# Kernel optimization log

Measured on AMD Instinct MI355X. Metric: run time of the kernel, lower is better.

## Reference

```python
import jax, jax.numpy as jnp
import numpy as np

GRID = 1024   # grid side -> V = GRID^2 verts
BATCH = 8     # homogeneous batch of meshes


def _grid_mesh_faces(S):
    # Triangulated regular grid: 2 triangles per cell.
    idx = np.arange(S * S, dtype=np.int64).reshape(S, S)
    a = idx[:-1, :-1].ravel()
    b = a + 1
    c = a + S
    d = a + S + 1
    f1 = np.stack([a, b, c], axis=1)
    f2 = np.stack([b, d, c], axis=1)
    return np.concatenate([f1, f2], axis=0)  # (F, 3) int64


def _unique_edges(faces, V):
    # Edge k of a face is opposite vertex k (pytorch3d convention):
    # edges = [(v1,v2), (v0,v2), (v0,v1)]
    e = np.stack([faces[:, [1, 2]], faces[:, [0, 2]], faces[:, [0, 1]]], axis=1)  # (F,3,2)
    e = np.sort(e, axis=-1)
    keys = e[..., 0] * np.int64(V) + e[..., 1]
    uniq, inv = np.unique(keys.ravel(), return_inverse=True)
    edges = np.stack([uniq // V, uniq % V], axis=1).astype(np.int64)  # (E,2)
    face_to_edge = inv.reshape(-1, 3).astype(np.int64)                # (F,3)
    return edges, face_to_edge


def setup_inputs() -> dict:
    key = jax.random.key(0)
    V = GRID * GRID
    faces_np = _grid_mesh_faces(GRID)
    edges_np, fte_np = _unique_edges(faces_np, V)
    verts = jax.random.normal(key, (BATCH, V, 3), dtype=jnp.float32)
    return {
        "verts": verts,
        "faces": jnp.asarray(faces_np),
        "edges": jnp.asarray(edges_np),
        "face_to_edge": jnp.asarray(fte_np),
    }


def reference(verts, faces, edges, face_to_edge):
    # verts: (N, V, 3); faces: (F, 3); edges: (E, 2); face_to_edge: (F, 3)
    N, V, _ = verts.shape
    # Gather edge endpoints and average to midpoints: (N, E, 2, 3) -> (N, E, 3)
    mid = verts[:, edges].mean(axis=2)
    # New verts = original verts followed by edge midpoints
    new_verts = jnp.concatenate([verts, mid], axis=1)  # (N, V+E, 3)
    # New faces (pytorch3d SubdivideMeshes._subdivide_faces ordering):
    e = face_to_edge + V  # midpoint vertex indices
    f0 = jnp.stack([faces[:, 0], e[:, 2], e[:, 1]], axis=1)
    f1 = jnp.stack([faces[:, 1], e[:, 0], e[:, 2]], axis=1)
    f2 = jnp.stack([faces[:, 2], e[:, 1], e[:, 0]], axis=1)
    f3 = e
    new_faces = jnp.concatenate([f0, f1, f2, f3], axis=0)  # (4F, 3)
    return new_verts, new_faces
```

## Files before the change

### kernel.cpp

```cpp
#include <hip/hip_runtime.h>
#include <stdint.h>


#define GRID_S 1024
#define V_CONST (GRID_S * GRID_S)

typedef float f4v __attribute__((ext_vector_type(4)));
typedef float f2v __attribute__((ext_vector_type(2)));

__global__ void copy_verts_k(const float* __restrict__ verts,
                             float* __restrict__ out,
                             int perBatch,
                             int rowStride3) {
    const int n = blockIdx.y;
    const int d0 = n * rowStride3;
    const float* __restrict__ src = verts + n * perBatch;
    float* __restrict__ dst = out + d0;

    const int pad = (4 - (d0 & 3)) & 3;
    const int main4 = (perBatch - pad) >> 2;
    const int k = blockIdx.x * blockDim.x + threadIdx.x;

    if (k < main4) {
        const int s = pad + (k << 2);
        f4v v;
        if (pad == 0) {
            v = *reinterpret_cast<const f4v*>(src + s);
        } else {
            v[0] = src[s + 0];
            v[1] = src[s + 1];
            v[2] = src[s + 2];
            v[3] = src[s + 3];
        }
        __builtin_nontemporal_store(v, reinterpret_cast<f4v*>(dst + s));
    }
    if (k == 0) {
        const int rem = (perBatch - pad) & 3;
        for (int i = 0; i < pad; ++i) dst[i] = src[i];
        for (int i = perBatch - rem; i < perBatch; ++i) dst[i] = src[i];
    }
}

__global__ void midpoints_k(const float* __restrict__ verts,
                            const int2* __restrict__ edges,
                            float* __restrict__ out,
                            int E, int N, int rowStride3) {
    const int e = blockIdx.x * blockDim.x + threadIdx.x;
    if (e >= E) return;
    const int2 ed = edges[e];
    const int i0 = 3 * ed.x;
    const int i1 = 3 * ed.y;

    const float* __restrict__ b = verts;
    float* __restrict__ o = out + (V_CONST + e) * 3;

#pragma unroll 2
    for (int n = 0; n < N; ++n) {
        const float x = 0.5f * (b[i0 + 0] + b[i1 + 0]);
        const float y = 0.5f * (b[i0 + 1] + b[i1 + 1]);
        const float z = 0.5f * (b[i0 + 2] + b[i1 + 2]);
        __builtin_nontemporal_store(x, o + 0);
        __builtin_nontemporal_store(y, o + 1);
        __builtin_nontemporal_store(z, o + 2);
        b += V_CONST * 3;
        o += rowStride3;
    }
}

__device__ __forceinline__ void store12(float* p, f4v w0, f4v w1, f4v w2) {
    const uintptr_t a = (uintptr_t)p;
    if ((a & 15) == 0) {
        f4v* q = reinterpret_cast<f4v*>(p);
        __builtin_nontemporal_store(w0, q + 0);
        __builtin_nontemporal_store(w1, q + 1);
        __builtin_nontemporal_store(w2, q + 2);
    } else if ((a & 7) == 0) {
        f2v* q = reinterpret_cast<f2v*>(p);
        f2v a0 = {w0[0], w0[1]}, a1 = {w0[2], w0[3]};
        f2v a2 = {w1[0], w1[1]}, a3 = {w1[2], w1[3]};
        f2v a4 = {w2[0], w2[1]}, a5 = {w2[2], w2[3]};
        __builtin_nontemporal_store(a0, q + 0);
        __builtin_nontemporal_store(a1, q + 1);
        __builtin_nontemporal_store(a2, q + 2);
        __builtin_nontemporal_store(a3, q + 3);
        __builtin_nontemporal_store(a4, q + 4);
        __builtin_nontemporal_store(a5, q + 5);
    } else {
#pragma unroll
        for (int i = 0; i < 4; ++i) __builtin_nontemporal_store(w0[i], p + i);
#pragma unroll
        for (int i = 0; i < 4; ++i) __builtin_nontemporal_store(w1[i], p + 4 + i);
#pragma unroll
        for (int i = 0; i < 4; ++i) __builtin_nontemporal_store(w2[i], p + 8 + i);
    }
}

__global__ void faces_k(const int* __restrict__ faces,
                        const int* __restrict__ fte,
                        float* __restrict__ out,
                        int F, int baseOut) {
    const int t = blockIdx.x * blockDim.x + threadIdx.x;
    const int mainT = F >> 2;
    float* __restrict__ base = out + baseOut;

    if (t < mainT) {
        const int4* f4 = reinterpret_cast<const int4*>(faces) + 3 * t;
        const int4* q4 = reinterpret_cast<const int4*>(fte) + 3 * t;
        const int4 p0 = f4[0], p1 = f4[1], p2 = f4[2];
        const int4 q0 = q4[0], q1 = q4[1], q2 = q4[2];

        const float a0 = (float)p0.x, a1 = (float)p0.w, a2 = (float)p1.z, a3 = (float)p2.y;
        const float b0 = (float)p0.y, b1 = (float)p1.x, b2 = (float)p1.w, b3 = (float)p2.z;
        const float c0 = (float)p0.z, c1 = (float)p1.y, c2 = (float)p2.x, c3 = (float)p2.w;

        const float e00 = (float)(q0.x + V_CONST), e01 = (float)(q0.w + V_CONST),
                    e02 = (float)(q1.z + V_CONST), e03 = (float)(q2.y + V_CONST);
        const float e10 = (float)(q0.y + V_CONST), e11 = (float)(q1.x + V_CONST),
                    e12 = (float)(q1.w + V_CONST), e13 = (float)(q2.z + V_CONST);
        const float e20 = (float)(q0.z + V_CONST), e21 = (float)(q1.y + V_CONST),
                    e22 = (float)(q2.x + V_CONST), e23 = (float)(q2.w + V_CONST);

        const int off = 12 * t;
        const int segF = 3 * F;

        store12(base + off,
                (f4v){a0, e20, e10, a1}, (f4v){e21, e11, a2, e22}, (f4v){e12, a3, e23, e13});
        store12(base + segF + off,
                (f4v){b0, e00, e20, b1}, (f4v){e01, e21, b2, e02}, (f4v){e22, b3, e03, e23});
        store12(base + 2 * segF + off,
                (f4v){c0, e10, e00, c1}, (f4v){e11, e01, c2, e12}, (f4v){e02, c3, e13, e03});
        store12(base + 3 * segF + off,
                (f4v){e00, e10, e20, e01}, (f4v){e11, e21, e02, e12}, (f4v){e22, e03, e13, e23});
    } else if (t == mainT) {
        for (int f = mainT * 4; f < F; ++f) {
            const int a = faces[3 * f + 0];
            const int b = faces[3 * f + 1];
            const int c = faces[3 * f + 2];
            const int e0 = fte[3 * f + 0] + V_CONST;
            const int e1 = fte[3 * f + 1] + V_CONST;
            const int e2 = fte[3 * f + 2] + V_CONST;
            float* o0 = base + 3 * f;
            float* o1 = o0 + 3 * F;
            float* o2 = o1 + 3 * F;
            float* o3 = o2 + 3 * F;
            o0[0] = (float)a;  o0[1] = (float)e2; o0[2] = (float)e1;
            o1[0] = (float)b;  o1[1] = (float)e0; o1[2] = (float)e2;
            o2[0] = (float)c;  o2[1] = (float)e1; o2[2] = (float)e0;
            o3[0] = (float)e0; o3[1] = (float)e1; o3[2] = (float)e2;
        }
    }
}

extern "C" void kernel_launch(void* const* d_in, const int* in_sizes, int n_in,
                              void* d_out, int out_size, void* d_ws, size_t ws_size,
                              hipStream_t stream) {
    const float* verts = (const float*)d_in[0];
    const int* faces   = (const int*)d_in[1];
    const int* edges   = (const int*)d_in[2];
    const int* fte     = (const int*)d_in[3];
    float* out = (float*)d_out;

    const int F = in_sizes[1] / 3;
    const int E = in_sizes[2] / 2;
    const int N = in_sizes[0] / (V_CONST * 3);

    const int perBatch   = V_CONST * 3;
    const int rowStride3 = (V_CONST + E) * 3;
    const int baseOut    = N * rowStride3;

    {
        dim3 block(256);
        dim3 grid((perBatch / 4 + 255) / 256, N);
        copy_verts_k<<<grid, block, 0, stream>>>(verts, out, perBatch, rowStride3);
    }
    {
        dim3 block(256);
        dim3 grid((E + 255) / 256);
        midpoints_k<<<grid, block, 0, stream>>>(verts, (const int2*)edges, out,
                                                E, N, rowStride3);
    }
    {
        const int mainT = F >> 2;
        dim3 block(256);
        dim3 grid((mainT + 1 + 255) / 256);
        faces_k<<<grid, block, 0, stream>>>(faces, fte, out, F, baseOut);
    }
}
```

Measured before the change: 655.2 us.

## Fuse copy, midpoint, and face kernels into one launch; use regular stores

Merges the three separate kernels (vertex copy, edge midpoints, face generation) into one launch that picks its role from block index ranges. This removes two launch gaps and lets the three phases run at the same time on the GPU. It also replaces the nontemporal stores with ordinary stores, which changes how the large output writes interact with the cache. The risk is losing the streaming-store behaviour on roughly a gigabyte of output writes.

```diff
diff --git a/kernel.cpp b/kernel.cpp
--- a/kernel.cpp
+++ b/kernel.cpp
@@ -4,102 +4,98 @@
 
 #define GRID_S 1024
 #define V_CONST (GRID_S * GRID_S)
+#define PER_BATCH (V_CONST * 3)
+#define CHUNKS_PER_BATCH (PER_BATCH / 4 / 256)
 
 typedef float f4v __attribute__((ext_vector_type(4)));
 typedef float f2v __attribute__((ext_vector_type(2)));
-
-__global__ void copy_verts_k(const float* __restrict__ verts,
-                             float* __restrict__ out,
-                             int perBatch,
-                             int rowStride3) {
-    const int n = blockIdx.y;
-    const int d0 = n * rowStride3;
-    const float* __restrict__ src = verts + n * perBatch;
-    float* __restrict__ dst = out + d0;
-
-    const int pad = (4 - (d0 & 3)) & 3;
-    const int main4 = (perBatch - pad) >> 2;
-    const int k = blockIdx.x * blockDim.x + threadIdx.x;
-
-    if (k < main4) {
-        const int s = pad + (k << 2);
-        f4v v;
-        if (pad == 0) {
-            v = *reinterpret_cast<const f4v*>(src + s);
-        } else {
-            v[0] = src[s + 0];
-            v[1] = src[s + 1];
-            v[2] = src[s + 2];
-            v[3] = src[s + 3];
-        }
-        __builtin_nontemporal_store(v, reinterpret_cast<f4v*>(dst + s));
-    }
-    if (k == 0) {
-        const int rem = (perBatch - pad) & 3;
-        for (int i = 0; i < pad; ++i) dst[i] = src[i];
-        for (int i = perBatch - rem; i < perBatch; ++i) dst[i] = src[i];
-    }
-}
-
-__global__ void midpoints_k(const float* __restrict__ verts,
-                            const int2* __restrict__ edges,
-                            float* __restrict__ out,
-                            int E, int N, int rowStride3) {
-    const int e = blockIdx.x * blockDim.x + threadIdx.x;
-    if (e >= E) return;
-    const int2 ed = edges[e];
-    const int i0 = 3 * ed.x;
-    const int i1 = 3 * ed.y;
-
-    const float* __restrict__ b = verts;
-    float* __restrict__ o = out + (V_CONST + e) * 3;
-
-#pragma unroll 2
-    for (int n = 0; n < N; ++n) {
-        const float x = 0.5f * (b[i0 + 0] + b[i1 + 0]);
-        const float y = 0.5f * (b[i0 + 1] + b[i1 + 1]);
-        const float z = 0.5f * (b[i0 + 2] + b[i1 + 2]);
-        __builtin_nontemporal_store(x, o + 0);
-        __builtin_nontemporal_store(y, o + 1);
-        __builtin_nontemporal_store(z, o + 2);
-        b += V_CONST * 3;
-        o += rowStride3;
-    }
-}
 
 __device__ __forceinline__ void store12(float* p, f4v w0, f4v w1, f4v w2) {
     const uintptr_t a = (uintptr_t)p;
     if ((a & 15) == 0) {
         f4v* q = reinterpret_cast<f4v*>(p);
-        __builtin_nontemporal_store(w0, q + 0);
-        __builtin_nontemporal_store(w1, q + 1);
-        __builtin_nontemporal_store(w2, q + 2);
+        q[0] = w0; q[1] = w1; q[2] = w2;
     } else if ((a & 7) == 0) {
         f2v* q = reinterpret_cast<f2v*>(p);
-        f2v a0 = {w0[0], w0[1]}, a1 = {w0[2], w0[3]};
-        f2v a2 = {w1[0], w1[1]}, a3 = {w1[2], w1[3]};
-        f2v a4 = {w2[0], w2[1]}, a5 = {w2[2], w2[3]};
-        __builtin_nontemporal_store(a0, q + 0);
-        __builtin_nontemporal_store(a1, q + 1);
-        __builtin_nontemporal_store(a2, q + 2);
-        __builtin_nontemporal_store(a3, q + 3);
-        __builtin_nontemporal_store(a4, q + 4);
-        __builtin_nontemporal_store(a5, q + 5);
+        q[0] = (f2v){w0[0], w0[1]};
+        q[1] = (f2v){w0[2], w0[3]};
+        q[2] = (f2v){w1[0], w1[1]};
+        q[3] = (f2v){w1[2], w1[3]};
+        q[4] = (f2v){w2[0], w2[1]};
+        q[5] = (f2v){w2[2], w2[3]};
     } else {
 #pragma unroll
-        for (int i = 0; i < 4; ++i) __builtin_nontemporal_store(w0[i], p + i);
+        for (int i = 0; i < 4; ++i) p[i] = w0[i];
 #pragma unroll
-        for (int i = 0; i < 4; ++i) __builtin_nontemporal_store(w1[i], p + 4 + i);
+        for (int i = 0; i < 4; ++i) p[4 + i] = w1[i];
 #pragma unroll
-        for (int i = 0; i < 4; ++i) __builtin_nontemporal_store(w2[i], p + 8 + i);
+        for (int i = 0; i < 4; ++i) p[8 + i] = w2[i];
     }
 }
 
-__global__ void faces_k(const int* __restrict__ faces,
-                        const int* __restrict__ fte,
-                        float* __restrict__ out,
-                        int F, int baseOut) {
-    const int t = blockIdx.x * blockDim.x + threadIdx.x;
+__global__ __launch_bounds__(256) void fused_k(
+    const float* __restrict__ verts,
+    const int2*  __restrict__ edges,
+    const int*   __restrict__ faces,
+    const int*   __restrict__ fte,
+    float* __restrict__ out,
+    int E, int F, int N, int rowStride3, int baseOut,
+    int Bcopy, int Bmid) {
+
+    const int b = blockIdx.x;
+    const int tid = threadIdx.x;
+
+    if (b < Bcopy) {
+        const int n  = b / CHUNKS_PER_BATCH;
+        const int cb = b - n * CHUNKS_PER_BATCH;
+        const int d0 = n * rowStride3;
+        const float* __restrict__ src = verts + n * PER_BATCH;
+        float* __restrict__ dst = out + d0;
+        const int pad = (4 - (d0 & 3)) & 3;
+        const int main4 = (PER_BATCH - pad) >> 2;
+        const int k = cb * 256 + tid;
+        if (k < main4) {
+            const int s = pad + (k << 2);
+            f4v v;
+            if (pad == 0) {
+                v = *reinterpret_cast<const f4v*>(src + s);
+            } else {
+                v[0] = src[s + 0];
+                v[1] = src[s + 1];
+                v[2] = src[s + 2];
+                v[3] = src[s + 3];
+            }
+            *reinterpret_cast<f4v*>(dst + s) = v;
+        }
+        if (k == 0) {
+            const int rem = (PER_BATCH - pad) & 3;
+            for (int i = 0; i < pad; ++i) dst[i] = src[i];
+            for (int i = PER_BATCH - rem; i < PER_BATCH; ++i) dst[i] = src[i];
+        }
+        return;
+    }
+
+    if (b < Bcopy + Bmid) {
+        const int e = (b - Bcopy) * 256 + tid;
+        if (e >= E) return;
+        const int2 ed = edges[e];
+        const int i0 = 3 * ed.x;
+        const int i1 = 3 * ed.y;
+        const float* __restrict__ vb = verts;
+        float* __restrict__ o = out + (V_CONST + e) * 3;
+#pragma unroll 2
+        for (int n = 0; n < N; ++n) {
+            const float x = 0.5f * (vb[i0 + 0] + vb[i1 + 0]);
+            const float y = 0.5f * (vb[i0 + 1] + vb[i1 + 1]);
+            const float z = 0.5f * (vb[i0 + 2] + vb[i1 + 2]);
+            o[0] = x; o[1] = y; o[2] = z;
+            vb += PER_BATCH;
+            o  += rowStride3;
+        }
+        return;
+    }
+
+    const int t = (b - Bcopy - Bmid) * 256 + tid;
     const int mainT = F >> 2;
     float* __restrict__ base = out + baseOut;
 
@@ -134,7 +130,7 @@
     } else if (t == mainT) {
         for (int f = mainT * 4; f < F; ++f) {
             const int a = faces[3 * f + 0];
-            const int b = faces[3 * f + 1];
+            const int bb = faces[3 * f + 1];
             const int c = faces[3 * f + 2];
             const int e0 = fte[3 * f + 0] + V_CONST;
             const int e1 = fte[3 * f + 1] + V_CONST;
@@ -144,7 +140,7 @@
             float* o2 = o1 + 3 * F;
             float* o3 = o2 + 3 * F;
             o0[0] = (float)a;  o0[1] = (float)e2; o0[2] = (float)e1;
-            o1[0] = (float)b;  o1[1] = (float)e0; o1[2] = (float)e2;
+            o1[0] = (float)bb; o1[1] = (float)e0; o1[2] = (float)e2;
             o2[0] = (float)c;  o2[1] = (float)e1; o2[2] = (float)e0;
             o3[0] = (float)e0; o3[1] = (float)e1; o3[2] = (float)e2;
         }
@@ -164,25 +160,15 @@
     const int E = in_sizes[2] / 2;
     const int N = in_sizes[0] / (V_CONST * 3);
 
-    const int perBatch   = V_CONST * 3;
     const int rowStride3 = (V_CONST + E) * 3;
     const int baseOut    = N * rowStride3;
 
-    {
-        dim3 block(256);
-        dim3 grid((perBatch / 4 + 255) / 256, N);
-        copy_verts_k<<<grid, block, 0, stream>>>(verts, out, perBatch, rowStride3);
-    }
-    {
-        dim3 block(256);
-        dim3 grid((E + 255) / 256);
-        midpoints_k<<<grid, block, 0, stream>>>(verts, (const int2*)edges, out,
-                                                E, N, rowStride3);
-    }
-    {
-        const int mainT = F >> 2;
-        dim3 block(256);
-        dim3 grid((mainT + 1 + 255) / 256);
-        faces_k<<<grid, block, 0, stream>>>(faces, fte, out, F, baseOut);
-    }
+    const int Bcopy = N * CHUNKS_PER_BATCH;
+    const int Bmid  = (E + 255) / 256;
+    const int Bfac  = ((F >> 2) + 1 + 255) / 256;
+    const int blocks = Bcopy + Bmid + Bfac;
+
+    fused_k<<<blocks, 256, 0, stream>>>(verts, (const int2*)edges, faces, fte,
+                                        out, E, F, N, rowStride3, baseOut,
+                                        Bcopy, Bmid);
 }
```

After: 650.1 us. No clear change (-0.8%).
